# Optimization experiments

Hardware: AMD Instinct MI355X
Metric: run time of the kernel (lower is better)

The kernel has to match this reference:

```python
import jax, jax.numpy as jnp
import numpy as np

N_NODES = 50000
N_EDGES = 800000
NFEAT = 128
NHID = 128
NCLASS = 10
NUM_GRAPHS = 512


def setup_inputs() -> dict:
    key = jax.random.key(0)
    ks = jax.random.split(key, 12)
    x = jax.random.normal(ks[0], (N_NODES, NFEAT), dtype=jnp.float32)
    edge_index = jax.random.randint(ks[1], (2, N_EDGES), 0, N_NODES, dtype=jnp.int64)
    batch = jnp.sort(jax.random.randint(ks[2], (N_NODES,), 0, NUM_GRAPHS, dtype=jnp.int64))
    def glorot(k, fan_in, fan_out):
        lim = np.sqrt(6.0 / (fan_in + fan_out))
        return jax.random.uniform(k, (fan_in, fan_out), jnp.float32, -lim, lim)
    return {
        "x": x, "edge_index": edge_index, "batch": batch,
        "W0": glorot(ks[3], NFEAT, NHID), "b0": jnp.zeros((NHID,), jnp.float32),
        "W1": glorot(ks[4], NHID, NHID), "b1": jnp.zeros((NHID,), jnp.float32),
        "W2": glorot(ks[5], NHID, NHID), "b2": jnp.zeros((NHID,), jnp.float32),
        "lin_w": glorot(ks[6], NHID, NCLASS), "lin_b": jnp.zeros((NCLASS,), jnp.float32),
    }


def _gcn_norm(edge_index, n):
    # PyG GCNConv: add self-loops, symmetric normalization D^-1/2 A D^-1/2
    loop = jnp.arange(n, dtype=edge_index.dtype)
    src = jnp.concatenate([edge_index[0], loop])  # [E+N]
    dst = jnp.concatenate([edge_index[1], loop])
    deg = jax.ops.segment_sum(jnp.ones_like(dst, dtype=jnp.float32), dst, num_segments=n)
    dis = jnp.where(deg > 0, jax.lax.rsqrt(jnp.maximum(deg, 1.0)), 0.0)
    norm = dis[src] * dis[dst]  # [E+N]
    return src, dst, norm


def _gcn_conv(x, W, b, src, dst, norm, n):
    h = x @ W                              # [N, nhid]
    msg = h[src] * norm[:, None]           # gather + scale, [E+N, nhid]
    out = jax.ops.segment_sum(msg, dst, num_segments=n)
    return out + b


def reference(x, edge_index, batch, W0, b0, W1, b1, W2, b2, lin_w, lin_b):
    n = x.shape[0]
    src, dst, norm = _gcn_norm(edge_index, n)
    h = x
    for (W, b) in ((W0, b0), (W1, b1), (W2, b2)):
        h = jax.nn.relu(_gcn_conv(h, W, b, src, dst, norm, n))
    # global mean pool over graphs
    sums = jax.ops.segment_sum(h, batch, num_segments=NUM_GRAPHS)
    cnts = jax.ops.segment_sum(jnp.ones((n,), jnp.float32), batch, num_segments=NUM_GRAPHS)
    pooled = sums / jnp.maximum(cnts, 1.0)[:, None]  # [G, nhid]
    logits = pooled @ lin_w + lin_b
    return jax.nn.log_softmax(logits, axis=-1)
```

## Files before the change

### kernel.cpp

```cpp
#include <hip/hip_runtime.h>
#include <hip/hip_fp16.h>


#define FEAT 128
#define NCLASS 10
#define NB_MAX 512

typedef _Float16 h8 __attribute__((ext_vector_type(8)));
typedef float f4 __attribute__((ext_vector_type(4)));

__global__ void __launch_bounds__(256) hist_wt_kernel(const int* __restrict__ ei,
                                                      int* __restrict__ bhist,
                                                      int ne, int nb, int epb, int hb,
                                                      const float* __restrict__ W0,
                                                      const float* __restrict__ W1,
                                                      const float* __restrict__ W2,
                                                      _Float16* __restrict__ Wt) {
  int t = threadIdx.x;
  if (blockIdx.x >= hb) {
    int i = (blockIdx.x - hb) * 256 + t;
    if (i < 3 * FEAT * FEAT) {
      int l = i / (FEAT * FEAT);
      int r = i - l * (FEAT * FEAT);
      int nn = r >> 7, kk = r & 127;
      const float* W = (l == 0) ? W0 : (l == 1) ? W1 : W2;
      Wt[i] = (_Float16)W[kk * FEAT + nn];
    }
    return;
  }
  __shared__ int lh[NB_MAX];
  for (int i = t; i < nb; i += 256) lh[i] = 0;
  __syncthreads();
  int r0 = blockIdx.x * epb;
  int r1 = min(r0 + epb, ne);
  for (int k = r0 + t; k < r1; k += 256) atomicAdd(&lh[ei[ne + k] >> 7], 1);
  __syncthreads();
  for (int i = t; i < nb; i += 256)
    if (lh[i]) atomicAdd(&bhist[i], lh[i]);
}

__global__ void __launch_bounds__(512) bscan_kernel(const int* __restrict__ bhist,
                                                    int* __restrict__ bstart,
                                                    int* __restrict__ bcur,
                                                    int* __restrict__ off,
                                                    int nb, int n, int ne) {
  __shared__ int sh[512];
  int t = threadIdx.x;
  int v = (t < nb) ? bhist[t] : 0;
  sh[t] = v;
  __syncthreads();
  int x = v;
  for (int d = 1; d < 512; d <<= 1) {
    int y = (t >= d) ? sh[t - d] : 0;
    __syncthreads();
    x += y;
    sh[t] = x;
    __syncthreads();
  }
  if (t < nb) {
    bstart[t] = x - v;
    bcur[t] = x - v;
  }
  if (t == 0) {
    bstart[nb] = ne;
    off[n] = ne;
  }
}

__global__ void __launch_bounds__(256) scatter_kernel(const int* __restrict__ ei,
                                                      int* __restrict__ bcur,
                                                      unsigned* __restrict__ buf,
                                                      int ne, int nb, int epb) {
  __shared__ int lh[NB_MAX], lbs[NB_MAX];
  int t = threadIdx.x;
  for (int i = t; i < nb; i += 256) lh[i] = 0;
  __syncthreads();
  int r0 = blockIdx.x * epb;
  int r1 = min(r0 + epb, ne);
  for (int k = r0 + t; k < r1; k += 256) atomicAdd(&lh[ei[ne + k] >> 7], 1);
  __syncthreads();
  for (int i = t; i < nb; i += 256) {
    int c = lh[i];
    lbs[i] = c ? atomicAdd(&bcur[i], c) : 0;
    lh[i] = 0;
  }
  __syncthreads();
  for (int k = r0 + t; k < r1; k += 256) {
    int src = ei[k];
    int dst = ei[ne + k];
    int b = dst >> 7;
    int p = lbs[b] + atomicAdd(&lh[b], 1);
    buf[p] = (unsigned)src | ((unsigned)(dst & 127) << 25);
  }
}

__global__ void __launch_bounds__(256) bucket_build_kernel(const unsigned* __restrict__ buf,
                                                           const int* __restrict__ bstart,
                                                           int* __restrict__ off,
                                                           int* __restrict__ csr,
                                                           float* __restrict__ dis, int n) {
  __shared__ int cnt[128], cur[128], sh[128];
  int b = blockIdx.x, t = threadIdx.x;
  int e0 = bstart[b], e1 = bstart[b + 1];
  if (t < 128) cnt[t] = 0;
  __syncthreads();
  for (int k = e0 + t; k < e1; k += 256) atomicAdd(&cnt[buf[k] >> 25], 1);
  __syncthreads();
  int v = (t < 128) ? cnt[t] : 0;
  if (t < 128) sh[t] = v;
  __syncthreads();
  int x = v;
  for (int d = 1; d < 128; d <<= 1) {
    int y = (t < 128 && t >= d) ? sh[t - d] : 0;
    __syncthreads();
    if (t < 128) {
      x += y;
      sh[t] = x;
    }
    __syncthreads();
  }
  if (t < 128) {
    int node = (b << 7) + t;
    cur[t] = x - v;
    if (node < n) {
      off[node] = e0 + x - v;
      dis[node] = rsqrtf((float)(v + 1));
    }
  }
  __syncthreads();
  for (int k = e0 + t; k < e1; k += 256) {
    unsigned u = buf[k];
    int d = u >> 25;
    int p = atomicAdd(&cur[d], 1);
    csr[e0 + p] = (int)(u & 0x1FFFFFFu);
  }
}

template <bool F32IN>
__global__ void __launch_bounds__(256) gemm_mfma_kernel(const void* __restrict__ Xin,
                                                        const _Float16* __restrict__ Wt,
                                                        const float* __restrict__ dis,
                                                        _Float16* __restrict__ Hs, int n) {
  __shared__ _Float16 st[64 * FEAT];
  int tid = threadIdx.x;
  int w = tid >> 6, lane = tid & 63;
  int l15 = lane & 15, hi = lane >> 4;

  int rowA = blockIdx.x * 64 + w * 16 + l15;
  int rA = min(rowA, n - 1);
  const _Float16* Xh = (const _Float16*)Xin;
  const float* Xf = (const float*)Xin;

  f4 acc[8];
#pragma unroll
  for (int nb = 0; nb < 8; ++nb) acc[nb] = (f4)(0.f);

#pragma unroll
  for (int kk = 0; kk < FEAT; kk += 32) {
    int ko = kk + hi * 8;
    h8 a;
    if (F32IN) {
      float4 x0 = *(const float4*)&Xf[(size_t)rA * FEAT + ko];
      float4 x1 = *(const float4*)&Xf[(size_t)rA * FEAT + ko + 4];
      a[0] = (_Float16)x0.x; a[1] = (_Float16)x0.y; a[2] = (_Float16)x0.z; a[3] = (_Float16)x0.w;
      a[4] = (_Float16)x1.x; a[5] = (_Float16)x1.y; a[6] = (_Float16)x1.z; a[7] = (_Float16)x1.w;
    } else {
      a = *(const h8*)&Xh[(size_t)rA * FEAT + ko];
    }
#pragma unroll
    for (int nb = 0; nb < 8; ++nb) {
      h8 bfr = *(const h8*)&Wt[(nb * 16 + l15) * FEAT + ko];
      acc[nb] = __builtin_amdgcn_mfma_f32_16x16x32_f16(a, bfr, acc[nb], 0, 0, 0);
    }
  }

  float dv[4];
#pragma unroll
  for (int r = 0; r < 4; ++r) {
    int grow = blockIdx.x * 64 + w * 16 + hi * 4 + r;
    dv[r] = dis[min(grow, n - 1)];
  }
#pragma unroll
  for (int nb = 0; nb < 8; ++nb)
#pragma unroll
    for (int r = 0; r < 4; ++r)
      st[(w * 16 + hi * 4 + r) * FEAT + nb * 16 + l15] = (_Float16)(acc[nb][r] * dv[r]);
  __syncthreads();

  int rowbase = blockIdx.x * 64;
#pragma unroll
  for (int i = tid; i < 64 * FEAT / 8; i += 256) {
    int row = rowbase + (i >> 4);
    if (row < n)
      *(uint4*)&Hs[(size_t)row * FEAT + (i & 15) * 8] =
          *(const uint4*)&st[(i >> 4) * FEAT + (i & 15) * 8];
  }
}

__global__ void __launch_bounds__(256) agg_kernel(const h8* __restrict__ Hs,
                                                  const int* __restrict__ csr,
                                                  const int* __restrict__ off,
                                                  const float* __restrict__ dis,
                                                  const float* __restrict__ b,
                                                  h8* __restrict__ out, int n) {
  int wave = threadIdx.x >> 6;
  int lane = threadIdx.x & 63;
  int grp = lane >> 4, lig = lane & 15;
  int node = blockIdx.x * 4 + wave;
  if (node >= n) return;
  int s = off[node];
  int e = off[node + 1];

  float acc[8];
  if (grp == 0) {
    h8 v = Hs[(size_t)node * 16 + lig];
#pragma unroll
    for (int j = 0; j < 8; ++j) acc[j] = (float)v[j];
  } else {
#pragma unroll
    for (int j = 0; j < 8; ++j) acc[j] = 0.f;
  }

  for (int k = s; k < e; k += 16) {
    int k0 = k + grp, k1 = k0 + 4, k2 = k0 + 8, k3 = k0 + 12;
    int i0 = (k0 < e) ? csr[k0] : -1;
    int i1 = (k1 < e) ? csr[k1] : -1;
    int i2 = (k2 < e) ? csr[k2] : -1;
    int i3 = (k3 < e) ? csr[k3] : -1;
    h8 v0 = Hs[(size_t)max(i0, 0) * 16 + lig];
    h8 v1 = Hs[(size_t)max(i1, 0) * 16 + lig];
    h8 v2 = Hs[(size_t)max(i2, 0) * 16 + lig];
    h8 v3 = Hs[(size_t)max(i3, 0) * 16 + lig];
    if (i0 >= 0) {
#pragma unroll
      for (int j = 0; j < 8; ++j) acc[j] += (float)v0[j];
    }
    if (i1 >= 0) {
#pragma unroll
      for (int j = 0; j < 8; ++j) acc[j] += (float)v1[j];
    }
    if (i2 >= 0) {
#pragma unroll
      for (int j = 0; j < 8; ++j) acc[j] += (float)v2[j];
    }
    if (i3 >= 0) {
#pragma unroll
      for (int j = 0; j < 8; ++j) acc[j] += (float)v3[j];
    }
  }

#pragma unroll
  for (int j = 0; j < 8; ++j) {
    acc[j] += __shfl_xor(acc[j], 16);
    acc[j] += __shfl_xor(acc[j], 32);
  }

  if (grp == 0) {
    float d = dis[node];
    float4 b0 = ((const float4*)b)[lig * 2];
    float4 b1 = ((const float4*)b)[lig * 2 + 1];
    h8 o;
    o[0] = (_Float16)fmaxf(fmaf(d, acc[0], b0.x), 0.f);
    o[1] = (_Float16)fmaxf(fmaf(d, acc[1], b0.y), 0.f);
    o[2] = (_Float16)fmaxf(fmaf(d, acc[2], b0.z), 0.f);
    o[3] = (_Float16)fmaxf(fmaf(d, acc[3], b0.w), 0.f);
    o[4] = (_Float16)fmaxf(fmaf(d, acc[4], b1.x), 0.f);
    o[5] = (_Float16)fmaxf(fmaf(d, acc[5], b1.y), 0.f);
    o[6] = (_Float16)fmaxf(fmaf(d, acc[6], b1.z), 0.f);
    o[7] = (_Float16)fmaxf(fmaf(d, acc[7], b1.w), 0.f);
    out[(size_t)node * 16 + lig] = o;
  }
}

__global__ void bounds_kernel(const int* __restrict__ batch, int* __restrict__ gstart,
                              int n, int g) {
  int i = blockIdx.x * 256 + threadIdx.x;
  if (i >= n) return;
  int bi = batch[i];
  int bp = (i == 0) ? -1 : batch[i - 1];
  for (int q = bp + 1; q <= bi; ++q) gstart[q] = i;
  if (i == n - 1) {
    for (int q = bi + 1; q <= g; ++q) gstart[q] = n;
  }
}

__global__ void __launch_bounds__(128) pool_kernel(const __half* __restrict__ h,
                                                   const int* __restrict__ gstart,
                                                   const float* __restrict__ lw,
                                                   const float* __restrict__ lb,
                                                   float* __restrict__ out) {
  int g = blockIdx.x;
  int t = threadIdx.x;
  int s = gstart[g];
  int e = gstart[g + 1];
  float a0 = 0.f, a1 = 0.f, a2 = 0.f, a3 = 0.f;
  int i = s;
  for (; i + 4 <= e; i += 4) {
    a0 += __half2float(h[(size_t)i * FEAT + t]);
    a1 += __half2float(h[(size_t)(i + 1) * FEAT + t]);
    a2 += __half2float(h[(size_t)(i + 2) * FEAT + t]);
    a3 += __half2float(h[(size_t)(i + 3) * FEAT + t]);
  }
  for (; i < e; ++i) a0 += __half2float(h[(size_t)i * FEAT + t]);
  float acc = a0 + a1 + a2 + a3;
  float cnt = (float)(e - s);
  float pooled = acc / fmaxf(cnt, 1.f);
  __shared__ float lds[FEAT];
  __shared__ float logits[NCLASS];
  lds[t] = pooled;
  __syncthreads();
  if (t < NCLASS) {
    float z = lb[t];
    for (int k = 0; k < FEAT; ++k) z += lds[k] * lw[k * NCLASS + t];
    logits[t] = z;
  }
  __syncthreads();
  if (t < NCLASS) {
    float m = logits[0];
#pragma unroll
    for (int c = 1; c < NCLASS; ++c) m = fmaxf(m, logits[c]);
    float ssum = 0.f;
#pragma unroll
    for (int c = 0; c < NCLASS; ++c) ssum += expf(logits[c] - m);
    out[(size_t)g * NCLASS + t] = logits[t] - m - logf(ssum);
  }
}

extern "C" void kernel_launch(void* const* d_in, const int* in_sizes, int n_in,
                              void* d_out, int out_size, void* d_ws, size_t ws_size,
                              hipStream_t stream) {
  const float* x = (const float*)d_in[0];
  const int* ei = (const int*)d_in[1];
  const int* batch = (const int*)d_in[2];
  const float* W0 = (const float*)d_in[3];
  const float* b0 = (const float*)d_in[4];
  const float* W1 = (const float*)d_in[5];
  const float* b1 = (const float*)d_in[6];
  const float* W2 = (const float*)d_in[7];
  const float* b2 = (const float*)d_in[8];
  const float* lw = (const float*)d_in[9];
  const float* lb = (const float*)d_in[10];

  int n = in_sizes[2];
  int ne = in_sizes[1] / 2;
  int g = out_size / NCLASS;
  int nb = (n + 127) >> 7;
  int hblocks = 120;
  int epb = (ne + hblocks - 1) / hblocks;
  int wtblocks = (3 * FEAT * FEAT + 255) / 256;

  char* ws = (char*)d_ws;
  size_t p = 0;
  auto alloc = [&](size_t bytes) {
    size_t cur = p;
    p += (bytes + 255) & ~(size_t)255;
    return cur;
  };
  int* off = (int*)(ws + alloc((size_t)(n + 1) * 4));
  int* csr = (int*)(ws + alloc((size_t)ne * 4));
  int* bhist = (int*)(ws + alloc((size_t)NB_MAX * 4));
  int* bstart = (int*)(ws + alloc((size_t)(NB_MAX + 1) * 4));
  int* bcur = (int*)(ws + alloc((size_t)NB_MAX * 4));
  int* gstart = (int*)(ws + alloc((size_t)(g + 1) * 4));
  float* dis = (float*)(ws + alloc((size_t)n * 4));
  unsigned* buf = (unsigned*)(ws + alloc((size_t)ne * 4));
  _Float16* Wt = (_Float16*)(ws + alloc((size_t)3 * FEAT * FEAT * 2));
  _Float16* Hs = (_Float16*)(ws + alloc((size_t)n * FEAT * 2));
  _Float16* Hb = (_Float16*)(ws + alloc((size_t)n * FEAT * 2));

  hipMemsetAsync(bhist, 0, NB_MAX * 4, stream);

  hist_wt_kernel<<<hblocks + wtblocks, 256, 0, stream>>>(ei, bhist, ne, nb, epb, hblocks,
                                                         W0, W1, W2, Wt);
  bscan_kernel<<<1, 512, 0, stream>>>(bhist, bstart, bcur, off, nb, n, ne);
  scatter_kernel<<<hblocks, 256, 0, stream>>>(ei, bcur, buf, ne, nb, epb);
  bucket_build_kernel<<<nb, 256, 0, stream>>>(buf, bstart, off, csr, dis, n);

  const float* bv[3] = {b0, b1, b2};
  for (int l = 0; l < 3; ++l) {
    const void* in = (l == 0) ? (const void*)x : (const void*)Hb;
    const _Float16* wt = Wt + (size_t)l * FEAT * FEAT;
    if (l == 0)
      gemm_mfma_kernel<true><<<(n + 63) / 64, 256, 0, stream>>>(in, wt, dis, Hs, n);
    else
      gemm_mfma_kernel<false><<<(n + 63) / 64, 256, 0, stream>>>(in, wt, dis, Hs, n);
    agg_kernel<<<(n + 3) / 4, 256, 0, stream>>>((const h8*)Hs, csr, off, dis, bv[l],
                                                (h8*)Hb, n);
  }

  bounds_kernel<<<(n + 255) / 256, 256, 0, stream>>>(batch, gstart, n, g);
  pool_kernel<<<g, 128, 0, stream>>>((const __half*)Hb, gstart, lw, lb, (float*)d_out);
}
```

Before: 222.5 us.

## Fuse aggregation of layer l with GEMM of layer l+1 in one kernel

Adds a fused kernel that gathers neighbour rows for 64 nodes, applies norm, bias and ReLU, and stages the result in swizzled LDS. It then runs the next layer's MFMA GEMM on that tile and writes the pre-scaled output. This removes two intermediate global round-trips and two kernel launches across the three layers. In exchange, each block has only 4 waves doing gather work over 64 nodes sequentially, which may reduce latency hiding compared to the old one-wave-per-node agg kernel.

```diff
diff --git a/kernel.cpp b/kernel.cpp
--- a/kernel.cpp
+++ b/kernel.cpp
@@ -8,6 +8,8 @@
 
 typedef _Float16 h8 __attribute__((ext_vector_type(8)));
 typedef float f4 __attribute__((ext_vector_type(4)));
+
+__device__ inline int swz(int row, int cbyte) { return row * 256 + (cbyte ^ ((row & 7) << 4)); }
 
 __global__ void __launch_bounds__(256) hist_wt_kernel(const int* __restrict__ ei,
                                                       int* __restrict__ bhist,
@@ -197,6 +199,109 @@
   }
 }
 
+__global__ void __launch_bounds__(256) fused_kernel(const h8* __restrict__ Hs_in,
+                                                    const int* __restrict__ csr,
+                                                    const int* __restrict__ off,
+                                                    const float* __restrict__ dis,
+                                                    const float* __restrict__ bias,
+                                                    const _Float16* __restrict__ Wt,
+                                                    _Float16* __restrict__ Hs_out, int n) {
+  __shared__ char xsb[64 * 256];
+  int tid = threadIdx.x;
+  int w = tid >> 6, lane = tid & 63;
+  int grp = lane >> 4, lig = lane & 15;
+  int row0 = blockIdx.x * 64;
+  int g16 = w * 4 + grp;
+
+  float4 b0 = ((const float4*)bias)[lig * 2];
+  float4 b1 = ((const float4*)bias)[lig * 2 + 1];
+  float bb[8] = {b0.x, b0.y, b0.z, b0.w, b1.x, b1.y, b1.z, b1.w};
+
+  for (int m = 0; m < 4; ++m) {
+    int ar = g16 * 4 + m;
+    int nd = min(row0 + ar, n - 1);
+    int s = off[nd], e = off[nd + 1];
+    float a0[8], a1[8], a2[8], a3[8];
+    h8 v = Hs_in[(size_t)nd * 16 + lig];
+#pragma unroll
+    for (int j = 0; j < 8; ++j) {
+      a0[j] = (float)v[j];
+      a1[j] = a2[j] = a3[j] = 0.f;
+    }
+    for (int k = s; k < e; k += 4) {
+      int i0 = csr[k];
+      int i1 = (k + 1 < e) ? csr[k + 1] : -1;
+      int i2 = (k + 2 < e) ? csr[k + 2] : -1;
+      int i3 = (k + 3 < e) ? csr[k + 3] : -1;
+      h8 v0 = Hs_in[(size_t)i0 * 16 + lig];
+      h8 v1 = Hs_in[(size_t)max(i1, 0) * 16 + lig];
+      h8 v2 = Hs_in[(size_t)max(i2, 0) * 16 + lig];
+      h8 v3 = Hs_in[(size_t)max(i3, 0) * 16 + lig];
+#pragma unroll
+      for (int j = 0; j < 8; ++j) a0[j] += (float)v0[j];
+      if (i1 >= 0) {
+#pragma unroll
+        for (int j = 0; j < 8; ++j) a1[j] += (float)v1[j];
+      }
+      if (i2 >= 0) {
+#pragma unroll
+        for (int j = 0; j < 8; ++j) a2[j] += (float)v2[j];
+      }
+      if (i3 >= 0) {
+#pragma unroll
+        for (int j = 0; j < 8; ++j) a3[j] += (float)v3[j];
+      }
+    }
+    float d = dis[nd];
+    h8 o;
+#pragma unroll
+    for (int j = 0; j < 8; ++j) {
+      float sum = a0[j] + a1[j] + a2[j] + a3[j];
+      o[j] = (_Float16)fmaxf(fmaf(d, sum, bb[j]), 0.f);
+    }
+    *(h8*)(xsb + swz(ar, lig * 16)) = o;
+  }
+  __syncthreads();
+
+  int l15 = lane & 15, hi = lane >> 4;
+  f4 acc[8];
+#pragma unroll
+  for (int nb = 0; nb < 8; ++nb) acc[nb] = (f4)(0.f);
+#pragma unroll
+  for (int kk = 0; kk < FEAT; kk += 32) {
+    int ko = kk + hi * 8;
+    h8 a = *(const h8*)(xsb + swz(w * 16 + l15, ko * 2));
+#pragma unroll
+    for (int nb = 0; nb < 8; ++nb) {
+      h8 bfr = *(const h8*)&Wt[(nb * 16 + l15) * FEAT + ko];
+      acc[nb] = __builtin_amdgcn_mfma_f32_16x16x32_f16(a, bfr, acc[nb], 0, 0, 0);
+    }
+  }
+
+  float dv[4];
+#pragma unroll
+  for (int r = 0; r < 4; ++r) {
+    int grow = row0 + w * 16 + hi * 4 + r;
+    dv[r] = dis[min(grow, n - 1)];
+  }
+  __syncthreads();
+#pragma unroll
+  for (int nb = 0; nb < 8; ++nb)
+#pragma unroll
+    for (int r = 0; r < 4; ++r) {
+      int srow = w * 16 + hi * 4 + r;
+      *(_Float16*)(xsb + swz(srow, (nb * 16 + l15) * 2)) = (_Float16)(acc[nb][r] * dv[r]);
+    }
+  __syncthreads();
+#pragma unroll
+  for (int i = tid; i < 64 * FEAT / 8; i += 256) {
+    int row = row0 + (i >> 4);
+    if (row < n)
+      *(uint4*)&Hs_out[(size_t)row * FEAT + (i & 15) * 8] =
+          *(const uint4*)(xsb + swz(i >> 4, (i & 15) * 16));
+  }
+}
+
 __global__ void __launch_bounds__(256) agg_kernel(const h8* __restrict__ Hs,
                                                   const int* __restrict__ csr,
                                                   const int* __restrict__ off,
@@ -365,8 +470,8 @@
   float* dis = (float*)(ws + alloc((size_t)n * 4));
   unsigned* buf = (unsigned*)(ws + alloc((size_t)ne * 4));
   _Float16* Wt = (_Float16*)(ws + alloc((size_t)3 * FEAT * FEAT * 2));
-  _Float16* Hs = (_Float16*)(ws + alloc((size_t)n * FEAT * 2));
-  _Float16* Hb = (_Float16*)(ws + alloc((size_t)n * FEAT * 2));
+  _Float16* HA = (_Float16*)(ws + alloc((size_t)n * FEAT * 2));
+  _Float16* HB = (_Float16*)(ws + alloc((size_t)n * FEAT * 2));
 
   hipMemsetAsync(bhist, 0, NB_MAX * 4, stream);
 
@@ -376,18 +481,14 @@
   scatter_kernel<<<hblocks, 256, 0, stream>>>(ei, bcur, buf, ne, nb, epb);
   bucket_build_kernel<<<nb, 256, 0, stream>>>(buf, bstart, off, csr, dis, n);
 
-  const float* bv[3] = {b0, b1, b2};
-  for (int l = 0; l < 3; ++l) {
-    const void* in = (l == 0) ? (const void*)x : (const void*)Hb;
-    const _Float16* wt = Wt + (size_t)l * FEAT * FEAT;
-    if (l == 0)
-      gemm_mfma_kernel<true><<<(n + 63) / 64, 256, 0, stream>>>(in, wt, dis, Hs, n);
-    else
-      gemm_mfma_kernel<false><<<(n + 63) / 64, 256, 0, stream>>>(in, wt, dis, Hs, n);
-    agg_kernel<<<(n + 3) / 4, 256, 0, stream>>>((const h8*)Hs, csr, off, dis, bv[l],
-                                                (h8*)Hb, n);
-  }
+  int gblocks = (n + 63) / 64;
+  gemm_mfma_kernel<true><<<gblocks, 256, 0, stream>>>(x, Wt, dis, HA, n);
+  fused_kernel<<<gblocks, 256, 0, stream>>>((const h8*)HA, csr, off, dis, b0,
+                                            Wt + (size_t)1 * FEAT * FEAT, HB, n);
+  fused_kernel<<<gblocks, 256, 0, stream>>>((const h8*)HB, csr, off, dis, b1,
+                                            Wt + (size_t)2 * FEAT * FEAT, HA, n);
+  agg_kernel<<<(n + 3) / 4, 256, 0, stream>>>((const h8*)HA, csr, off, dis, b2, (h8*)HB, n);
 
   bounds_kernel<<<(n + 255) / 256, 256, 0, stream>>>(batch, gstart, n, g);
-  pool_kernel<<<g, 128, 0, stream>>>((const __half*)Hb, gstart, lw, lb, (float*)d_out);
-}
+  pool_kernel<<<g, 128, 0, stream>>>((const __half*)HB, gstart, lw, lb, (float*)d_out);
+}
```

Result: faster. 209.4 us (-5.9%).
